# Kernel optimization log

Measured on AMD Instinct MI355X. Metric: run time of the kernel, lower is better.

## Reference

```python
import jax, jax.numpy as jnp
import numpy as np

B, S, D = 2, 2048, 1024
H = 2048          # expert hidden size; up-proj width is 2*H (GLU)
E = 8             # num_experts
K = 2             # top_k


def setup_inputs() -> dict:
    key = jax.random.key(0)
    k1, k2, k3, k4, k5 = jax.random.split(key, 5)
    x = jax.random.normal(k1, (B, S, D), dtype=jnp.float32)
    expert_p = jax.random.uniform(k2, (B, S, K), dtype=jnp.float32)
    expert_idxs = jax.random.randint(k3, (B, S, K), 0, E)
    W1 = jax.random.normal(k4, (E, D, 2 * H), dtype=jnp.float32) * 0.02
    W2 = jax.random.normal(k5, (E, H, D), dtype=jnp.float32) * 0.02
    return {"x": x, "expert_p": expert_p, "expert_idxs": expert_idxs, "W1": W1, "W2": W2}


def reference(x, expert_p, expert_idxs, W1, W2):
    # x: [B, S, D]; expert_p/expert_idxs: [B, S, K]; W1: [E, D, 2H]; W2: [E, H, D]
    x_shape = x.shape
    d = x_shape[-1]
    k = expert_idxs.shape[-1]
    n_experts = W1.shape[0]
    xf = x.reshape(-1, d)                      # [T, D]
    T = xf.shape[0]
    e_flat = expert_idxs.reshape(-1)           # [P] token-major pair order, P = T*k
    xp = jnp.repeat(xf, k, axis=0)             # [P, D] matches e_flat ordering

    # Grouped up-projection: each (token, expert) pair hits its expert's W1.
    up = jnp.zeros((T * k, W1.shape[-1]), dtype=x.dtype)
    for e in range(n_experts):                 # fixed small loop over experts
        up = up + jnp.where((e_flat == e)[:, None], xp @ W1[e], 0)

    # Fused GLU: chunk(2), exact GELU (torch nn.GELU default), gate (g + 1).
    h, g = jnp.split(up, 2, axis=-1)           # [P, H] each
    a = jax.nn.gelu(h, approximate=False) * (g + 1)

    # Grouped down-projection.
    down = jnp.zeros((T * k, d), dtype=x.dtype)
    for e in range(n_experts):
        down = down + jnp.where((e_flat == e)[:, None], a @ W2[e], 0)

    # Gated scatter-combine over the top_k pairs of each token.
    gates = expert_p.reshape(T, k)             # [T, K]
    y = jnp.sum(down.reshape(T, k, d) * gates[..., None], axis=1)
    return y.reshape(*x_shape[:-1], d)
```

## Files before the change

### kernel.cpp

```cpp
#include <hip/hip_runtime.h>
#include <hip/hip_bf16.h>
#include <math.h>

#define TT 4096
#define PP 8192
#define DD 1024
#define HH 2048
#define EE 8
#define CC1 4096

typedef __attribute__((ext_vector_type(8))) short s16x8;
typedef __attribute__((ext_vector_type(4))) float f32x4;

#define W1T_OFF   0ull
#define W2T_OFF   (W1T_OFF + (size_t)EE*DD*CC1*2)
#define XB_OFF    (W2T_OFF + (size_t)EE*HH*DD*2)
#define ABUF_OFF  (XB_OFF  + (size_t)TT*DD*2)
#define DOWN_OFF  (ABUF_OFF + (size_t)PP*HH*2)
#define META_OFF  (DOWN_OFF + (size_t)2*PP*DD*2)
#define PAIR_OFF  (META_OFF + 2048)
#define POS_OFF   (PAIR_OFF + (size_t)PP*4)

#define VMCNT(N) asm volatile("s_waitcnt vmcnt(" #N ")" ::: "memory")
#define CFENCE() asm volatile("" ::: "memory")

__device__ __forceinline__ unsigned short f2bf(float f) {
  union { float f; unsigned u; } a; a.f = f;
  unsigned u = a.u;
  unsigned r = u + 0x7FFFu + ((u >> 16) & 1u);
  return (unsigned short)(r >> 16);
}

__device__ __forceinline__ float bf2f(unsigned short s) {
  union { unsigned u; float f; } a; a.u = ((unsigned)s) << 16;
  return a.f;
}

__device__ __forceinline__ void gload16(const void* g, void* l) {
  __builtin_amdgcn_global_load_lds(
      (const __attribute__((address_space(1))) void*)(uintptr_t)g,
      (__attribute__((address_space(3))) void*)(unsigned)(uintptr_t)l,
      16, 0, 0);
}

__global__ void k_cvt_x(const float* __restrict__ in, unsigned short* __restrict__ out, int n4) {
  int i = blockIdx.x * blockDim.x + threadIdx.x;
  if (i >= n4) return;
  float4 v = reinterpret_cast<const float4*>(in)[i];
  ushort4 o;
  o.x = f2bf(v.x); o.y = f2bf(v.y); o.z = f2bf(v.z); o.w = f2bf(v.w);
  reinterpret_cast<ushort4*>(out)[i] = o;
}

__global__ __launch_bounds__(256) void k_transpose(const float* __restrict__ in,
                                                   unsigned short* __restrict__ out,
                                                   int R, int C) {
  __shared__ float t[64][65];
  const size_t mbase = (size_t)blockIdx.z * (size_t)R * (size_t)C;
  int c0 = blockIdx.x * 64, r0 = blockIdx.y * 64;
  int tid = threadIdx.x;
#pragma unroll
  for (int i = 0; i < 4; ++i) {
    int ch = tid + i * 256;
    int row = ch >> 4, c4 = (ch & 15) * 4;
    float4 v = *reinterpret_cast<const float4*>(&in[mbase + (size_t)(r0 + row) * C + c0 + c4]);
    t[row][c4] = v.x; t[row][c4 + 1] = v.y; t[row][c4 + 2] = v.z; t[row][c4 + 3] = v.w;
  }
  __syncthreads();
#pragma unroll
  for (int i = 0; i < 4; ++i) {
    int ch = tid + i * 256;
    int c = ch >> 4, rb = (ch & 15) * 4;
    ushort4 o;
    o.x = f2bf(t[rb][c]); o.y = f2bf(t[rb + 1][c]);
    o.z = f2bf(t[rb + 2][c]); o.w = f2bf(t[rb + 3][c]);
    *reinterpret_cast<ushort4*>(&out[mbase + (size_t)(c0 + c) * R + r0 + rb]) = o;
  }
}

__global__ void k_route(const int* __restrict__ eidx, int* __restrict__ meta,
                        int* __restrict__ plist, int* __restrict__ pos) {
  __shared__ int cnt[EE], off[EE + 1], cur[EE];
  int tid = threadIdx.x;
  if (tid < EE) { cnt[tid] = 0; cur[tid] = 0; }
  __syncthreads();
  for (int p = tid; p < PP; p += blockDim.x) atomicAdd(&cnt[eidx[p]], 1);
  __syncthreads();
  if (tid == 0) {
    int s = 0;
    for (int e = 0; e < EE; ++e) { off[e] = s; s += cnt[e]; }
    off[EE] = s;
    int n256 = 0;
    for (int e = 0; e < EE; ++e)
      for (int r = 0; r < cnt[e]; r += 256) {
        meta[16 + 2*n256] = e; meta[17 + 2*n256] = off[e] + r; ++n256;
      }
    meta[0] = n256;
    for (int e = 0; e <= EE; ++e) meta[1 + e] = off[e];
  }
  __syncthreads();
  for (int p = tid; p < PP; p += blockDim.x) {
    int e = eidx[p];
    int q = off[e] + atomicAdd(&cur[e], 1);
    plist[q] = p;
    pos[p] = q;
  }
}

__global__ __launch_bounds__(512) void k_gemm1(
    const unsigned short* __restrict__ xb,
    const unsigned short* __restrict__ w1t,
    const float* __restrict__ gates,
    const int* __restrict__ meta,
    const int* __restrict__ plist,
    unsigned short* __restrict__ abuf)
{
  const int nt = meta[0];
  const int tb = blockIdx.x;
  if (tb >= nt) return;
  const int e  = meta[16 + 2*tb];
  const int q0 = meta[17 + 2*tb];
  const int nrows = min(256, meta[2 + e] - q0);
  const int c0 = blockIdx.y * 64;

  __shared__ unsigned short As[3][256 * 64];
  __shared__ unsigned short Bs[3][128 * 64];

  const int tid = threadIdx.x;
  const int wave = tid >> 6, lane = tid & 63;
  const int l15 = lane & 15, l4 = lane >> 4;
  const int wr = wave >> 1, wc = wave & 1;

  const unsigned short* w1e = w1t + (size_t)e * CC1 * DD;

  const unsigned short* aga[4];
  const unsigned short* bga[2];
#pragma unroll
  for (int i = 0; i < 4; ++i) {
    int c = tid + i * 512;
    int row = c >> 3;
    int ko = ((c & 7) ^ (row & 7)) * 8;
    int r = row < nrows ? row : 0;
    int p = plist[q0 + r];
    aga[i] = xb + (size_t)(p >> 1) * DD + ko;
  }
#pragma unroll
  for (int i = 0; i < 2; ++i) {
    int c = tid + i * 512;
    int row = c >> 3;
    int ko = ((c & 7) ^ (row & 7)) * 8;
    int u = row & 63, wcq = row >> 6;
    int col = (u < 32) ? (c0 + wcq * 32 + u) : (HH + c0 + wcq * 32 + (u - 32));
    bga[i] = w1e + (size_t)col * DD + ko;
  }

  f32x4 acc[4][4];
#pragma unroll
  for (int a = 0; a < 4; ++a)
#pragma unroll
    for (int b = 0; b < 4; ++b) acc[a][b] = (f32x4)0.0f;

  auto stage = [&](int kk, unsigned short* pa, unsigned short* pb) {
#pragma unroll
    for (int i = 0; i < 4; ++i) gload16(aga[i] + kk, pa + (tid + i * 512) * 8);
#pragma unroll
    for (int i = 0; i < 2; ++i) gload16(bga[i] + kk, pb + (tid + i * 512) * 8);
  };

  auto compute_tile = [&](const unsigned short* sa, const unsigned short* sb) {
    const char* A8 = (const char*)sa;
    const char* B8 = (const char*)sb;
#pragma unroll
    for (int ks = 0; ks < 2; ++ks) {
      s16x8 af[4], bfr[4];
#pragma unroll
      for (int rf = 0; rf < 4; ++rf) {
        int row = wr * 64 + rf * 16 + l15;
        af[rf] = *(const s16x8*)(A8 + ((row * 128 + ks * 64 + l4 * 16) ^ ((row & 7) << 4)));
      }
#pragma unroll
      for (int cf = 0; cf < 4; ++cf) {
        int row = wc * 64 + cf * 16 + l15;
        bfr[cf] = *(const s16x8*)(B8 + ((row * 128 + ks * 64 + l4 * 16) ^ ((row & 7) << 4)));
      }
#pragma unroll
      for (int rf = 0; rf < 4; ++rf)
#pragma unroll
        for (int cf = 0; cf < 4; ++cf)
          acc[rf][cf] = __builtin_amdgcn_mfma_f32_16x16x32_bf16(af[rf], bfr[cf], acc[rf][cf], 0, 0, 0);
    }
  };

  unsigned short *a0 = As[0], *a1 = As[1], *a2 = As[2];
  unsigned short *b0 = Bs[0], *b1 = Bs[1], *b2 = Bs[2];

  stage(0, a0, b0);
  stage(64, a1, b1);
  VMCNT(6);
  __builtin_amdgcn_s_barrier();
  CFENCE();

  for (int kt = 0; kt < DD / 64 - 2; ++kt) {
    stage((kt + 2) * 64, a2, b2);
    compute_tile(a0, b0);
    VMCNT(6);
    __builtin_amdgcn_s_barrier();
    CFENCE();
    unsigned short* t;
    t = a0; a0 = a1; a1 = a2; a2 = t;
    t = b0; b0 = b1; b1 = b2; b2 = t;
  }
  compute_tile(a0, b0);
  VMCNT(0);
  __builtin_amdgcn_s_barrier();
  CFENCE();
  compute_tile(a1, b1);

#pragma unroll
  for (int rf = 0; rf < 4; ++rf) {
#pragma unroll
    for (int i = 0; i < 4; ++i) {
      int r = wr * 64 + rf * 16 + l4 * 4 + i;
      if (r < nrows) {
        int q = q0 + r;
        float gt = gates[plist[q]];
        unsigned short* orow = abuf + (size_t)q * HH + c0 + wc * 32 + l15;
#pragma unroll
        for (int cf = 0; cf < 2; ++cf) {
          float hv = acc[rf][cf][i];
          float gv = acc[rf][cf + 2][i];
          float av = 0.5f * hv * (1.0f + erff(hv * 0.70710678118654752f)) * (gv + 1.0f) * gt;
          orow[cf * 16] = f2bf(av);
        }
      }
    }
  }
}

__global__ __launch_bounds__(512) void k_gemm2(
    const unsigned short* __restrict__ abuf,
    const unsigned short* __restrict__ w2t,
    const int* __restrict__ meta,
    unsigned short* __restrict__ down)
{
  const int nt = meta[0];
  const int tb = blockIdx.x;
  if (tb >= nt) return;
  const int e  = meta[16 + 2*tb];
  const int q0 = meta[17 + 2*tb];
  const int nrows = min(256, meta[2 + e] - q0);
  const int c0 = blockIdx.y * 128;
  const int kz = blockIdx.z * (HH / 2);

  __shared__ unsigned short As[3][256 * 64];
  __shared__ unsigned short Bs[3][128 * 64];

  const int tid = threadIdx.x;
  const int wave = tid >> 6, lane = tid & 63;
  const int l15 = lane & 15, l4 = lane >> 4;
  const int wr = wave >> 1, wc = wave & 1;

  const unsigned short* w2e = w2t + (size_t)e * DD * HH;

  const unsigned short* aga[4];
  const unsigned short* bga[2];
#pragma unroll
  for (int i = 0; i < 4; ++i) {
    int c = tid + i * 512;
    int row = c >> 3;
    int ko = ((c & 7) ^ (row & 7)) * 8;
    int r = row < nrows ? row : 0;
    aga[i] = abuf + (size_t)(q0 + r) * HH + kz + ko;
  }
#pragma unroll
  for (int i = 0; i < 2; ++i) {
    int c = tid + i * 512;
    int row = c >> 3;
    int ko = ((c & 7) ^ (row & 7)) * 8;
    bga[i] = w2e + (size_t)(c0 + row) * HH + kz + ko;
  }

  f32x4 acc[4][4];
#pragma unroll
  for (int a = 0; a < 4; ++a)
#pragma unroll
    for (int b = 0; b < 4; ++b) acc[a][b] = (f32x4)0.0f;

  auto stage = [&](int kk, unsigned short* pa, unsigned short* pb) {
#pragma unroll
    for (int i = 0; i < 4; ++i) gload16(aga[i] + kk, pa + (tid + i * 512) * 8);
#pragma unroll
    for (int i = 0; i < 2; ++i) gload16(bga[i] + kk, pb + (tid + i * 512) * 8);
  };

  auto compute_tile = [&](const unsigned short* sa, const unsigned short* sb) {
    const char* A8 = (const char*)sa;
    const char* B8 = (const char*)sb;
#pragma unroll
    for (int ks = 0; ks < 2; ++ks) {
      s16x8 af[4], bfr[4];
#pragma unroll
      for (int rf = 0; rf < 4; ++rf) {
        int row = wr * 64 + rf * 16 + l15;
        af[rf] = *(const s16x8*)(A8 + ((row * 128 + ks * 64 + l4 * 16) ^ ((row & 7) << 4)));
      }
#pragma unroll
      for (int cf = 0; cf < 4; ++cf) {
        int row = wc * 64 + cf * 16 + l15;
        bfr[cf] = *(const s16x8*)(B8 + ((row * 128 + ks * 64 + l4 * 16) ^ ((row & 7) << 4)));
      }
#pragma unroll
      for (int rf = 0; rf < 4; ++rf)
#pragma unroll
        for (int cf = 0; cf < 4; ++cf)
          acc[rf][cf] = __builtin_amdgcn_mfma_f32_16x16x32_bf16(af[rf], bfr[cf], acc[rf][cf], 0, 0, 0);
    }
  };

  unsigned short *a0 = As[0], *a1 = As[1], *a2 = As[2];
  unsigned short *b0 = Bs[0], *b1 = Bs[1], *b2 = Bs[2];

  stage(0, a0, b0);
  stage(64, a1, b1);
  VMCNT(6);
  __builtin_amdgcn_s_barrier();
  CFENCE();

  const int NT = (HH / 2) / 64;
  for (int kt = 0; kt < NT - 2; ++kt) {
    stage((kt + 2) * 64, a2, b2);
    compute_tile(a0, b0);
    VMCNT(6);
    __builtin_amdgcn_s_barrier();
    CFENCE();
    unsigned short* t;
    t = a0; a0 = a1; a1 = a2; a2 = t;
    t = b0; b0 = b1; b1 = b2; b2 = t;
  }
  compute_tile(a0, b0);
  VMCNT(0);
  __builtin_amdgcn_s_barrier();
  CFENCE();
  compute_tile(a1, b1);

  unsigned short* dz = down + (size_t)blockIdx.z * PP * DD;
#pragma unroll
  for (int rf = 0; rf < 4; ++rf) {
#pragma unroll
    for (int i = 0; i < 4; ++i) {
      int r = wr * 64 + rf * 16 + l4 * 4 + i;
      if (r < nrows) {
        int q = q0 + r;
        unsigned short* orow = dz + (size_t)q * DD + c0 + wc * 64 + l15;
#pragma unroll
        for (int cf = 0; cf < 4; ++cf) orow[cf * 16] = f2bf(acc[rf][cf][i]);
      }
    }
  }
}

__global__ void k_combine(const unsigned short* __restrict__ down, const int* __restrict__ pos,
                          float* __restrict__ y) {
  int i = blockIdx.x * blockDim.x + threadIdx.x;
  if (i >= TT * DD / 8) return;
  int t = i >> 7;
  int c8 = (i & 127) * 8;
  int qa = pos[2 * t], qb = pos[2 * t + 1];
  const unsigned short* d0 = down;
  const unsigned short* d1 = down + (size_t)PP * DD;
  s16x8 va0 = *reinterpret_cast<const s16x8*>(d0 + (size_t)qa * DD + c8);
  s16x8 va1 = *reinterpret_cast<const s16x8*>(d1 + (size_t)qa * DD + c8);
  s16x8 vb0 = *reinterpret_cast<const s16x8*>(d0 + (size_t)qb * DD + c8);
  s16x8 vb1 = *reinterpret_cast<const s16x8*>(d1 + (size_t)qb * DD + c8);
  float o[8];
#pragma unroll
  for (int j = 0; j < 8; ++j)
    o[j] = bf2f((unsigned short)va0[j]) + bf2f((unsigned short)va1[j]) +
           bf2f((unsigned short)vb0[j]) + bf2f((unsigned short)vb1[j]);
  float4* yo = reinterpret_cast<float4*>(y + (size_t)t * DD + c8);
  yo[0] = (float4){o[0], o[1], o[2], o[3]};
  yo[1] = (float4){o[4], o[5], o[6], o[7]};
}

extern "C" void kernel_launch(void* const* d_in, const int* in_sizes, int n_in,
                              void* d_out, int out_size, void* d_ws, size_t ws_size,
                              hipStream_t stream) {
  const float* x  = (const float*)d_in[0];
  const float* ep = (const float*)d_in[1];
  const int*   ei = (const int*)d_in[2];
  const float* W1 = (const float*)d_in[3];
  const float* W2 = (const float*)d_in[4];
  float* y = (float*)d_out;
  char* ws = (char*)d_ws;

  unsigned short* w1t = (unsigned short*)(ws + W1T_OFF);
  unsigned short* w2t = (unsigned short*)(ws + W2T_OFF);
  unsigned short* xb  = (unsigned short*)(ws + XB_OFF);
  unsigned short* ab  = (unsigned short*)(ws + ABUF_OFF);
  unsigned short* down = (unsigned short*)(ws + DOWN_OFF);
  int* meta   = (int*)(ws + META_OFF);
  int* plist  = (int*)(ws + PAIR_OFF);
  int* pos    = (int*)(ws + POS_OFF);

  hipLaunchKernelGGL(k_cvt_x, dim3(TT * DD / 4 / 256), dim3(256), 0, stream,
                     x, xb, TT * DD / 4);
  hipLaunchKernelGGL(k_transpose, dim3(CC1 / 64, DD / 64, EE), dim3(256), 0, stream,
                     W1, w1t, DD, CC1);
  hipLaunchKernelGGL(k_transpose, dim3(DD / 64, HH / 64, EE), dim3(256), 0, stream,
                     W2, w2t, HH, DD);
  hipLaunchKernelGGL(k_route, dim3(1), dim3(256), 0, stream, ei, meta, plist, pos);
  hipLaunchKernelGGL(k_gemm1, dim3(40, 32), dim3(512), 0, stream,
                     xb, w1t, ep, meta, plist, ab);
  hipLaunchKernelGGL(k_gemm2, dim3(40, 8, 2), dim3(512), 0, stream,
                     ab, w2t, meta, down);
  hipLaunchKernelGGL(k_combine, dim3(TT * DD / 8 / 256), dim3(256), 0, stream,
                     down, pos, y);
}
```

Measured before the change: 270.1 us.

## Interleave LDS reads, global prefetch and MFMA in ping-pong phases with setprio

Both grouped GEMM kernels now split each K-tile into two half-phases. Each phase issues LDS fragment reads and half of the next tile's global-to-LDS loads, then waits at a barrier and on lgkmcnt before running 16 MFMAs under raised wave priority. The intent is a HipKittens-style ping-pong schedule in which some waves do memory work while others compute, keeping the matrix cores busier. It adds more barriers per tile, and the vmcnt(6) accounting must still line up with the split staging.

Result: no change. 275.0 us (+1.8%).

```diff
diff --git a/kernel.cpp b/kernel.cpp
--- a/kernel.cpp
+++ b/kernel.cpp
@@ -23,6 +23,8 @@
 
 #define VMCNT(N) asm volatile("s_waitcnt vmcnt(" #N ")" ::: "memory")
 #define CFENCE() asm volatile("" ::: "memory")
+#define LGKM0() do { asm volatile("s_waitcnt lgkmcnt(0)" ::: "memory"); \
+                     __builtin_amdgcn_sched_barrier(0); } while (0)
 
 __device__ __forceinline__ unsigned short f2bf(float f) {
   union { float f; unsigned u; } a; a.f = f;
@@ -160,61 +162,89 @@
 #pragma unroll
     for (int b = 0; b < 4; ++b) acc[a][b] = (f32x4)0.0f;
 
-  auto stage = [&](int kk, unsigned short* pa, unsigned short* pb) {
-#pragma unroll
-    for (int i = 0; i < 4; ++i) gload16(aga[i] + kk, pa + (tid + i * 512) * 8);
-#pragma unroll
-    for (int i = 0; i < 2; ++i) gload16(bga[i] + kk, pb + (tid + i * 512) * 8);
-  };
-
-  auto compute_tile = [&](const unsigned short* sa, const unsigned short* sb) {
+  auto stage_h0 = [&](int kk, unsigned short* pa, unsigned short* pb) {
+    gload16(aga[0] + kk, pa + (tid + 0 * 512) * 8);
+    gload16(aga[1] + kk, pa + (tid + 1 * 512) * 8);
+    gload16(bga[0] + kk, pb + (tid + 0 * 512) * 8);
+  };
+  auto stage_h1 = [&](int kk, unsigned short* pa, unsigned short* pb) {
+    gload16(aga[2] + kk, pa + (tid + 2 * 512) * 8);
+    gload16(aga[3] + kk, pa + (tid + 3 * 512) * 8);
+    gload16(bga[1] + kk, pb + (tid + 1 * 512) * 8);
+  };
+
+  auto dsread = [&](const unsigned short* sa, const unsigned short* sb, int ks,
+                    s16x8* af, s16x8* bfr) {
     const char* A8 = (const char*)sa;
     const char* B8 = (const char*)sb;
 #pragma unroll
-    for (int ks = 0; ks < 2; ++ks) {
-      s16x8 af[4], bfr[4];
-#pragma unroll
-      for (int rf = 0; rf < 4; ++rf) {
-        int row = wr * 64 + rf * 16 + l15;
-        af[rf] = *(const s16x8*)(A8 + ((row * 128 + ks * 64 + l4 * 16) ^ ((row & 7) << 4)));
-      }
-#pragma unroll
-      for (int cf = 0; cf < 4; ++cf) {
-        int row = wc * 64 + cf * 16 + l15;
-        bfr[cf] = *(const s16x8*)(B8 + ((row * 128 + ks * 64 + l4 * 16) ^ ((row & 7) << 4)));
-      }
-#pragma unroll
-      for (int rf = 0; rf < 4; ++rf)
-#pragma unroll
-        for (int cf = 0; cf < 4; ++cf)
-          acc[rf][cf] = __builtin_amdgcn_mfma_f32_16x16x32_bf16(af[rf], bfr[cf], acc[rf][cf], 0, 0, 0);
-    }
+    for (int rf = 0; rf < 4; ++rf) {
+      int row = wr * 64 + rf * 16 + l15;
+      af[rf] = *(const s16x8*)(A8 + ((row * 128 + ks * 64 + l4 * 16) ^ ((row & 7) << 4)));
+    }
+#pragma unroll
+    for (int cf = 0; cf < 4; ++cf) {
+      int row = wc * 64 + cf * 16 + l15;
+      bfr[cf] = *(const s16x8*)(B8 + ((row * 128 + ks * 64 + l4 * 16) ^ ((row & 7) << 4)));
+    }
+  };
+  auto mfma16 = [&](const s16x8* af, const s16x8* bfr) {
+    __builtin_amdgcn_s_setprio(1);
+#pragma unroll
+    for (int rf = 0; rf < 4; ++rf)
+#pragma unroll
+      for (int cf = 0; cf < 4; ++cf)
+        acc[rf][cf] = __builtin_amdgcn_mfma_f32_16x16x32_bf16(af[rf], bfr[cf], acc[rf][cf], 0, 0, 0);
+    __builtin_amdgcn_s_setprio(0);
   };
 
   unsigned short *a0 = As[0], *a1 = As[1], *a2 = As[2];
   unsigned short *b0 = Bs[0], *b1 = Bs[1], *b2 = Bs[2];
 
-  stage(0, a0, b0);
-  stage(64, a1, b1);
+  stage_h0(0, a0, b0);  stage_h1(0, a0, b0);
+  stage_h0(64, a1, b1); stage_h1(64, a1, b1);
   VMCNT(6);
   __builtin_amdgcn_s_barrier();
   CFENCE();
 
+  s16x8 af[4], bfr[4];
   for (int kt = 0; kt < DD / 64 - 2; ++kt) {
-    stage((kt + 2) * 64, a2, b2);
-    compute_tile(a0, b0);
+    const int kk = (kt + 2) * 64;
+    dsread(a0, b0, 0, af, bfr);
+    stage_h0(kk, a2, b2);
+    __builtin_amdgcn_s_barrier();
+    LGKM0();
+    mfma16(af, bfr);
+    __builtin_amdgcn_s_barrier();
+    dsread(a0, b0, 1, af, bfr);
+    stage_h1(kk, a2, b2);
     VMCNT(6);
+    __builtin_amdgcn_s_barrier();
+    LGKM0();
+    mfma16(af, bfr);
     __builtin_amdgcn_s_barrier();
     CFENCE();
     unsigned short* t;
     t = a0; a0 = a1; a1 = a2; a2 = t;
     t = b0; b0 = b1; b1 = b2; b2 = t;
   }
-  compute_tile(a0, b0);
+  dsread(a0, b0, 0, af, bfr);
+  __builtin_amdgcn_s_barrier();
+  LGKM0();
+  mfma16(af, bfr);
+  __builtin_amdgcn_s_barrier();
+  dsread(a0, b0, 1, af, bfr);
   VMCNT(0);
   __builtin_amdgcn_s_barrier();
-  CFENCE();
-  compute_tile(a1, b1);
+  LGKM0();
+  mfma16(af, bfr);
+  __builtin_amdgcn_s_barrier();
+  dsread(a1, b1, 0, af, bfr);
+  LGKM0();
+  mfma16(af, bfr);
+  dsread(a1, b1, 1, af, bfr);
+  LGKM0();
+  mfma16(af, bfr);
 
 #pragma unroll
   for (int rf = 0; rf < 4; ++rf) {
@@ -286,62 +316,89 @@
 #pragma unroll
     for (int b = 0; b < 4; ++b) acc[a][b] = (f32x4)0.0f;
 
-  auto stage = [&](int kk, unsigned short* pa, unsigned short* pb) {
-#pragma unroll
-    for (int i = 0; i < 4; ++i) gload16(aga[i] + kk, pa + (tid + i * 512) * 8);
-#pragma unroll
-    for (int i = 0; i < 2; ++i) gload16(bga[i] + kk, pb + (tid + i * 512) * 8);
-  };
-
-  auto compute_tile = [&](const unsigned short* sa, const unsigned short* sb) {
+  auto stage_h0 = [&](int kk, unsigned short* pa, unsigned short* pb) {
+    gload16(aga[0] + kk, pa + (tid + 0 * 512) * 8);
+    gload16(aga[1] + kk, pa + (tid + 1 * 512) * 8);
+    gload16(bga[0] + kk, pb + (tid + 0 * 512) * 8);
+  };
+  auto stage_h1 = [&](int kk, unsigned short* pa, unsigned short* pb) {
+    gload16(aga[2] + kk, pa + (tid + 2 * 512) * 8);
+    gload16(aga[3] + kk, pa + (tid + 3 * 512) * 8);
+    gload16(bga[1] + kk, pb + (tid + 1 * 512) * 8);
+  };
+  auto dsread = [&](const unsigned short* sa, const unsigned short* sb, int ks,
+                    s16x8* af, s16x8* bfr) {
     const char* A8 = (const char*)sa;
     const char* B8 = (const char*)sb;
 #pragma unroll
-    for (int ks = 0; ks < 2; ++ks) {
-      s16x8 af[4], bfr[4];
-#pragma unroll
-      for (int rf = 0; rf < 4; ++rf) {
-        int row = wr * 64 + rf * 16 + l15;
-        af[rf] = *(const s16x8*)(A8 + ((row * 128 + ks * 64 + l4 * 16) ^ ((row & 7) << 4)));
-      }
-#pragma unroll
-      for (int cf = 0; cf < 4; ++cf) {
-        int row = wc * 64 + cf * 16 + l15;
-        bfr[cf] = *(const s16x8*)(B8 + ((row * 128 + ks * 64 + l4 * 16) ^ ((row & 7) << 4)));
-      }
-#pragma unroll
-      for (int rf = 0; rf < 4; ++rf)
-#pragma unroll
-        for (int cf = 0; cf < 4; ++cf)
-          acc[rf][cf] = __builtin_amdgcn_mfma_f32_16x16x32_bf16(af[rf], bfr[cf], acc[rf][cf], 0, 0, 0);
-    }
+    for (int rf = 0; rf < 4; ++rf) {
+      int row = wr * 64 + rf * 16 + l15;
+      af[rf] = *(const s16x8*)(A8 + ((row * 128 + ks * 64 + l4 * 16) ^ ((row & 7) << 4)));
+    }
+#pragma unroll
+    for (int cf = 0; cf < 4; ++cf) {
+      int row = wc * 64 + cf * 16 + l15;
+      bfr[cf] = *(const s16x8*)(B8 + ((row * 128 + ks * 64 + l4 * 16) ^ ((row & 7) << 4)));
+    }
+  };
+  auto mfma16 = [&](const s16x8* af, const s16x8* bfr) {
+    __builtin_amdgcn_s_setprio(1);
+#pragma unroll
+    for (int rf = 0; rf < 4; ++rf)
+#pragma unroll
+      for (int cf = 0; cf < 4; ++cf)
+        acc[rf][cf] = __builtin_amdgcn_mfma_f32_16x16x32_bf16(af[rf], bfr[cf], acc[rf][cf], 0, 0, 0);
+    __builtin_amdgcn_s_setprio(0);
   };
 
   unsigned short *a0 = As[0], *a1 = As[1], *a2 = As[2];
   unsigned short *b0 = Bs[0], *b1 = Bs[1], *b2 = Bs[2];
 
-  stage(0, a0, b0);
-  stage(64, a1, b1);
+  stage_h0(0, a0, b0);  stage_h1(0, a0, b0);
+  stage_h0(64, a1, b1); stage_h1(64, a1, b1);
   VMCNT(6);
   __builtin_amdgcn_s_barrier();
   CFENCE();
 
+  s16x8 af[4], bfr[4];
   const int NT = (HH / 2) / 64;
   for (int kt = 0; kt < NT - 2; ++kt) {
-    stage((kt + 2) * 64, a2, b2);
-    compute_tile(a0, b0);
+    const int kk = (kt + 2) * 64;
+    dsread(a0, b0, 0, af, bfr);
+    stage_h0(kk, a2, b2);
+    __builtin_amdgcn_s_barrier();
+    LGKM0();
+    mfma16(af, bfr);
+    __builtin_amdgcn_s_barrier();
+    dsread(a0, b0, 1, af, bfr);
+    stage_h1(kk, a2, b2);
     VMCNT(6);
+    __builtin_amdgcn_s_barrier();
+    LGKM0();
+    mfma16(af, bfr);
     __builtin_amdgcn_s_barrier();
     CFENCE();
     unsigned short* t;
     t = a0; a0 = a1; a1 = a2; a2 = t;
     t = b0; b0 = b1; b1 = b2; b2 = t;
   }
-  compute_tile(a0, b0);
+  dsread(a0, b0, 0, af, bfr);
+  __builtin_amdgcn_s_barrier();
+  LGKM0();
+  mfma16(af, bfr);
+  __builtin_amdgcn_s_barrier();
+  dsread(a0, b0, 1, af, bfr);
   VMCNT(0);
   __builtin_amdgcn_s_barrier();
-  CFENCE();
-  compute_tile(a1, b1);
+  LGKM0();
+  mfma16(af, bfr);
+  __builtin_amdgcn_s_barrier();
+  dsread(a1, b1, 0, af, bfr);
+  LGKM0();
+  mfma16(af, bfr);
+  dsread(a1, b1, 1, af, bfr);
+  LGKM0();
+  mfma16(af, bfr);
 
   unsigned short* dz = down + (size_t)blockIdx.z * PP * DD;
 #pragma unroll
```

## Enlarge grouped-GEMM tiles to 256x256, double-buffer, and split down-proj K four ways

Applied to the files above, without the earlier changes.

Both expert GEMMs move from 256x128 to 256x256 output tiles, with each wave owning a 128x64 sub-tile. The goal is to raise arithmetic intensity and cut redundant global loads of the activation rows. The triple-buffered vmcnt-pipelined loop becomes a simpler double-buffered loop that uses __syncthreads, which can expose more load latency. The down-projection split-K goes from 2 to 4 so the grid size stays the same, and the combine kernel now sums four partials. To fit the larger partial buffer, it reuses the W1 transpose workspace after gemm1 has finished. The 128KB LDS per block and 128 accumulator floats per thread, together with launch_bounds(512,2), risk register spills and low occupancy.

New measurement: 282.9 us. 4.7% more time.

```diff
diff --git a/kernel.cpp b/kernel.cpp
--- a/kernel.cpp
+++ b/kernel.cpp
@@ -13,16 +13,13 @@
 typedef __attribute__((ext_vector_type(4))) float f32x4;
 
 #define W1T_OFF   0ull
+#define DOWN_OFF  W1T_OFF
 #define W2T_OFF   (W1T_OFF + (size_t)EE*DD*CC1*2)
 #define XB_OFF    (W2T_OFF + (size_t)EE*HH*DD*2)
 #define ABUF_OFF  (XB_OFF  + (size_t)TT*DD*2)
-#define DOWN_OFF  (ABUF_OFF + (size_t)PP*HH*2)
-#define META_OFF  (DOWN_OFF + (size_t)2*PP*DD*2)
+#define META_OFF  (ABUF_OFF + (size_t)PP*HH*2)
 #define PAIR_OFF  (META_OFF + 2048)
 #define POS_OFF   (PAIR_OFF + (size_t)PP*4)
-
-#define VMCNT(N) asm volatile("s_waitcnt vmcnt(" #N ")" ::: "memory")
-#define CFENCE() asm volatile("" ::: "memory")
 
 __device__ __forceinline__ unsigned short f2bf(float f) {
   union { float f; unsigned u; } a; a.f = f;
@@ -107,7 +104,7 @@
   }
 }
 
-__global__ __launch_bounds__(512) void k_gemm1(
+__global__ __launch_bounds__(512, 2) void k_gemm1(
     const unsigned short* __restrict__ xb,
     const unsigned short* __restrict__ w1t,
     const float* __restrict__ gates,
@@ -121,20 +118,20 @@
   const int e  = meta[16 + 2*tb];
   const int q0 = meta[17 + 2*tb];
   const int nrows = min(256, meta[2 + e] - q0);
-  const int c0 = blockIdx.y * 64;
-
-  __shared__ unsigned short As[3][256 * 64];
-  __shared__ unsigned short Bs[3][128 * 64];
+  const int c0 = blockIdx.y * 128;
+
+  __shared__ unsigned short As[2][256 * 64];
+  __shared__ unsigned short Bs[2][256 * 64];
 
   const int tid = threadIdx.x;
   const int wave = tid >> 6, lane = tid & 63;
   const int l15 = lane & 15, l4 = lane >> 4;
-  const int wr = wave >> 1, wc = wave & 1;
+  const int wm = wave >> 2, wn = wave & 3;
 
   const unsigned short* w1e = w1t + (size_t)e * CC1 * DD;
 
   const unsigned short* aga[4];
-  const unsigned short* bga[2];
+  const unsigned short* bga[4];
 #pragma unroll
   for (int i = 0; i < 4; ++i) {
     int c = tid + i * 512;
@@ -143,20 +140,14 @@
     int r = row < nrows ? row : 0;
     int p = plist[q0 + r];
     aga[i] = xb + (size_t)(p >> 1) * DD + ko;
-  }
-#pragma unroll
-  for (int i = 0; i < 2; ++i) {
-    int c = tid + i * 512;
-    int row = c >> 3;
-    int ko = ((c & 7) ^ (row & 7)) * 8;
-    int u = row & 63, wcq = row >> 6;
-    int col = (u < 32) ? (c0 + wcq * 32 + u) : (HH + c0 + wcq * 32 + (u - 32));
+    int b = row >> 4, u = row & 15;
+    int col = ((b & 1) ? HH : 0) + c0 + (b >> 1) * 16 + u;
     bga[i] = w1e + (size_t)col * DD + ko;
   }
 
-  f32x4 acc[4][4];
-#pragma unroll
-  for (int a = 0; a < 4; ++a)
+  f32x4 acc[8][4];
+#pragma unroll
+  for (int a = 0; a < 8; ++a)
 #pragma unroll
     for (int b = 0; b < 4; ++b) acc[a][b] = (f32x4)0.0f;
 
@@ -164,7 +155,7 @@
 #pragma unroll
     for (int i = 0; i < 4; ++i) gload16(aga[i] + kk, pa + (tid + i * 512) * 8);
 #pragma unroll
-    for (int i = 0; i < 2; ++i) gload16(bga[i] + kk, pb + (tid + i * 512) * 8);
+    for (int i = 0; i < 4; ++i) gload16(bga[i] + kk, pb + (tid + i * 512) * 8);
   };
 
   auto compute_tile = [&](const unsigned short* sa, const unsigned short* sb) {
@@ -172,72 +163,56 @@
     const char* B8 = (const char*)sb;
 #pragma unroll
     for (int ks = 0; ks < 2; ++ks) {
-      s16x8 af[4], bfr[4];
-#pragma unroll
-      for (int rf = 0; rf < 4; ++rf) {
-        int row = wr * 64 + rf * 16 + l15;
+      s16x8 af[8], bfr[4];
+#pragma unroll
+      for (int rf = 0; rf < 8; ++rf) {
+        int row = wm * 128 + rf * 16 + l15;
         af[rf] = *(const s16x8*)(A8 + ((row * 128 + ks * 64 + l4 * 16) ^ ((row & 7) << 4)));
       }
 #pragma unroll
       for (int cf = 0; cf < 4; ++cf) {
-        int row = wc * 64 + cf * 16 + l15;
+        int row = wn * 64 + cf * 16 + l15;
         bfr[cf] = *(const s16x8*)(B8 + ((row * 128 + ks * 64 + l4 * 16) ^ ((row & 7) << 4)));
       }
 #pragma unroll
-      for (int rf = 0; rf < 4; ++rf)
+      for (int rf = 0; rf < 8; ++rf)
 #pragma unroll
         for (int cf = 0; cf < 4; ++cf)
           acc[rf][cf] = __builtin_amdgcn_mfma_f32_16x16x32_bf16(af[rf], bfr[cf], acc[rf][cf], 0, 0, 0);
     }
   };
 
-  unsigned short *a0 = As[0], *a1 = As[1], *a2 = As[2];
-  unsigned short *b0 = Bs[0], *b1 = Bs[1], *b2 = Bs[2];
-
-  stage(0, a0, b0);
-  stage(64, a1, b1);
-  VMCNT(6);
-  __builtin_amdgcn_s_barrier();
-  CFENCE();
-
-  for (int kt = 0; kt < DD / 64 - 2; ++kt) {
-    stage((kt + 2) * 64, a2, b2);
-    compute_tile(a0, b0);
-    VMCNT(6);
-    __builtin_amdgcn_s_barrier();
-    CFENCE();
-    unsigned short* t;
-    t = a0; a0 = a1; a1 = a2; a2 = t;
-    t = b0; b0 = b1; b1 = b2; b2 = t;
-  }
-  compute_tile(a0, b0);
-  VMCNT(0);
-  __builtin_amdgcn_s_barrier();
-  CFENCE();
-  compute_tile(a1, b1);
-
-#pragma unroll
-  for (int rf = 0; rf < 4; ++rf) {
+  stage(0, As[0], Bs[0]);
+  __syncthreads();
+  const int NT = DD / 64;
+  for (int kt = 0; kt < NT; ++kt) {
+    if (kt + 1 < NT) stage((kt + 1) * 64, As[(kt + 1) & 1], Bs[(kt + 1) & 1]);
+    compute_tile(As[kt & 1], Bs[kt & 1]);
+    if (kt + 1 < NT) __syncthreads();
+  }
+
+#pragma unroll
+  for (int rf = 0; rf < 8; ++rf) {
 #pragma unroll
     for (int i = 0; i < 4; ++i) {
-      int r = wr * 64 + rf * 16 + l4 * 4 + i;
+      int r = wm * 128 + rf * 16 + l4 * 4 + i;
       if (r < nrows) {
         int q = q0 + r;
         float gt = gates[plist[q]];
-        unsigned short* orow = abuf + (size_t)q * HH + c0 + wc * 32 + l15;
-#pragma unroll
-        for (int cf = 0; cf < 2; ++cf) {
-          float hv = acc[rf][cf][i];
-          float gv = acc[rf][cf + 2][i];
+        unsigned short* orow = abuf + (size_t)q * HH + c0 + 2 * wn * 16 + l15;
+#pragma unroll
+        for (int j = 0; j < 2; ++j) {
+          float hv = acc[rf][2 * j][i];
+          float gv = acc[rf][2 * j + 1][i];
           float av = 0.5f * hv * (1.0f + erff(hv * 0.70710678118654752f)) * (gv + 1.0f) * gt;
-          orow[cf * 16] = f2bf(av);
+          orow[j * 16] = f2bf(av);
         }
       }
     }
   }
 }
 
-__global__ __launch_bounds__(512) void k_gemm2(
+__global__ __launch_bounds__(512, 2) void k_gemm2(
     const unsigned short* __restrict__ abuf,
     const unsigned short* __restrict__ w2t,
     const int* __restrict__ meta,
@@ -249,21 +224,21 @@
   const int e  = meta[16 + 2*tb];
   const int q0 = meta[17 + 2*tb];
   const int nrows = min(256, meta[2 + e] - q0);
-  const int c0 = blockIdx.y * 128;
-  const int kz = blockIdx.z * (HH / 2);
-
-  __shared__ unsigned short As[3][256 * 64];
-  __shared__ unsigned short Bs[3][128 * 64];
+  const int c0 = blockIdx.y * 256;
+  const int kz = blockIdx.z * (HH / 4);
+
+  __shared__ unsigned short As[2][256 * 64];
+  __shared__ unsigned short Bs[2][256 * 64];
 
   const int tid = threadIdx.x;
   const int wave = tid >> 6, lane = tid & 63;
   const int l15 = lane & 15, l4 = lane >> 4;
-  const int wr = wave >> 1, wc = wave & 1;
+  const int wm = wave >> 2, wn = wave & 3;
 
   const unsigned short* w2e = w2t + (size_t)e * DD * HH;
 
   const unsigned short* aga[4];
-  const unsigned short* bga[2];
+  const unsigned short* bga[4];
 #pragma unroll
   for (int i = 0; i < 4; ++i) {
     int c = tid + i * 512;
@@ -271,18 +246,12 @@
     int ko = ((c & 7) ^ (row & 7)) * 8;
     int r = row < nrows ? row : 0;
     aga[i] = abuf + (size_t)(q0 + r) * HH + kz + ko;
-  }
-#pragma unroll
-  for (int i = 0; i < 2; ++i) {
-    int c = tid + i * 512;
-    int row = c >> 3;
-    int ko = ((c & 7) ^ (row & 7)) * 8;
     bga[i] = w2e + (size_t)(c0 + row) * HH + kz + ko;
   }
 
-  f32x4 acc[4][4];
-#pragma unroll
-  for (int a = 0; a < 4; ++a)
+  f32x4 acc[8][4];
+#pragma unroll
+  for (int a = 0; a < 8; ++a)
 #pragma unroll
     for (int b = 0; b < 4; ++b) acc[a][b] = (f32x4)0.0f;
 
@@ -290,7 +259,7 @@
 #pragma unroll
     for (int i = 0; i < 4; ++i) gload16(aga[i] + kk, pa + (tid + i * 512) * 8);
 #pragma unroll
-    for (int i = 0; i < 2; ++i) gload16(bga[i] + kk, pb + (tid + i * 512) * 8);
+    for (int i = 0; i < 4; ++i) gload16(bga[i] + kk, pb + (tid + i * 512) * 8);
   };
 
   auto compute_tile = [&](const unsigned short* sa, const unsigned short* sb) {
@@ -298,60 +267,43 @@
     const char* B8 = (const char*)sb;
 #pragma unroll
     for (int ks = 0; ks < 2; ++ks) {
-      s16x8 af[4], bfr[4];
-#pragma unroll
-      for (int rf = 0; rf < 4; ++rf) {
-        int row = wr * 64 + rf * 16 + l15;
+      s16x8 af[8], bfr[4];
+#pragma unroll
+      for (int rf = 0; rf < 8; ++rf) {
+        int row = wm * 128 + rf * 16 + l15;
         af[rf] = *(const s16x8*)(A8 + ((row * 128 + ks * 64 + l4 * 16) ^ ((row & 7) << 4)));
       }
 #pragma unroll
       for (int cf = 0; cf < 4; ++cf) {
-        int row = wc * 64 + cf * 16 + l15;
+        int row = wn * 64 + cf * 16 + l15;
         bfr[cf] = *(const s16x8*)(B8 + ((row * 128 + ks * 64 + l4 * 16) ^ ((row & 7) << 4)));
       }
 #pragma unroll
-      for (int rf = 0; rf < 4; ++rf)
+      for (int rf = 0; rf < 8; ++rf)
 #pragma unroll
         for (int cf = 0; cf < 4; ++cf)
           acc[rf][cf] = __builtin_amdgcn_mfma_f32_16x16x32_bf16(af[rf], bfr[cf], acc[rf][cf], 0, 0, 0);
     }
   };
 
-  unsigned short *a0 = As[0], *a1 = As[1], *a2 = As[2];
-  unsigned short *b0 = Bs[0], *b1 = Bs[1], *b2 = Bs[2];
-
-  stage(0, a0, b0);
-  stage(64, a1, b1);
-  VMCNT(6);
-  __builtin_amdgcn_s_barrier();
-  CFENCE();
-
-  const int NT = (HH / 2) / 64;
-  for (int kt = 0; kt < NT - 2; ++kt) {
-    stage((kt + 2) * 64, a2, b2);
-    compute_tile(a0, b0);
-    VMCNT(6);
-    __builtin_amdgcn_s_barrier();
-    CFENCE();
-    unsigned short* t;
-    t = a0; a0 = a1; a1 = a2; a2 = t;
-    t = b0; b0 = b1; b1 = b2; b2 = t;
-  }
-  compute_tile(a0, b0);
-  VMCNT(0);
-  __builtin_amdgcn_s_barrier();
-  CFENCE();
-  compute_tile(a1, b1);
+  stage(0, As[0], Bs[0]);
+  __syncthreads();
+  const int NT = (HH / 4) / 64;
+  for (int kt = 0; kt < NT; ++kt) {
+    if (kt + 1 < NT) stage((kt + 1) * 64, As[(kt + 1) & 1], Bs[(kt + 1) & 1]);
+    compute_tile(As[kt & 1], Bs[kt & 1]);
+    if (kt + 1 < NT) __syncthreads();
+  }
 
   unsigned short* dz = down + (size_t)blockIdx.z * PP * DD;
 #pragma unroll
-  for (int rf = 0; rf < 4; ++rf) {
+  for (int rf = 0; rf < 8; ++rf) {
 #pragma unroll
     for (int i = 0; i < 4; ++i) {
-      int r = wr * 64 + rf * 16 + l4 * 4 + i;
+      int r = wm * 128 + rf * 16 + l4 * 4 + i;
       if (r < nrows) {
         int q = q0 + r;
-        unsigned short* orow = dz + (size_t)q * DD + c0 + wc * 64 + l15;
+        unsigned short* orow = dz + (size_t)q * DD + c0 + wn * 64 + l15;
 #pragma unroll
         for (int cf = 0; cf < 4; ++cf) orow[cf * 16] = f2bf(acc[rf][cf][i]);
       }
@@ -366,17 +318,18 @@
   int t = i >> 7;
   int c8 = (i & 127) * 8;
   int qa = pos[2 * t], qb = pos[2 * t + 1];
-  const unsigned short* d0 = down;
-  const unsigned short* d1 = down + (size_t)PP * DD;
-  s16x8 va0 = *reinterpret_cast<const s16x8*>(d0 + (size_t)qa * DD + c8);
-  s16x8 va1 = *reinterpret_cast<const s16x8*>(d1 + (size_t)qa * DD + c8);
-  s16x8 vb0 = *reinterpret_cast<const s16x8*>(d0 + (size_t)qb * DD + c8);
-  s16x8 vb1 = *reinterpret_cast<const s16x8*>(d1 + (size_t)qb * DD + c8);
   float o[8];
 #pragma unroll
-  for (int j = 0; j < 8; ++j)
-    o[j] = bf2f((unsigned short)va0[j]) + bf2f((unsigned short)va1[j]) +
-           bf2f((unsigned short)vb0[j]) + bf2f((unsigned short)vb1[j]);
+  for (int j = 0; j < 8; ++j) o[j] = 0.0f;
+#pragma unroll
+  for (int z = 0; z < 4; ++z) {
+    const unsigned short* dz = down + (size_t)z * PP * DD;
+    s16x8 va = *reinterpret_cast<const s16x8*>(dz + (size_t)qa * DD + c8);
+    s16x8 vb = *reinterpret_cast<const s16x8*>(dz + (size_t)qb * DD + c8);
+#pragma unroll
+    for (int j = 0; j < 8; ++j)
+      o[j] += bf2f((unsigned short)va[j]) + bf2f((unsigned short)vb[j]);
+  }
   float4* yo = reinterpret_cast<float4*>(y + (size_t)t * DD + c8);
   yo[0] = (float4){o[0], o[1], o[2], o[3]};
   yo[1] = (float4){o[4], o[5], o[6], o[7]};
@@ -409,9 +362,9 @@
   hipLaunchKernelGGL(k_transpose, dim3(DD / 64, HH / 64, EE), dim3(256), 0, stream,
                      W2, w2t, HH, DD);
   hipLaunchKernelGGL(k_route, dim3(1), dim3(256), 0, stream, ei, meta, plist, pos);
-  hipLaunchKernelGGL(k_gemm1, dim3(40, 32), dim3(512), 0, stream,
+  hipLaunchKernelGGL(k_gemm1, dim3(40, 16), dim3(512), 0, stream,
                      xb, w1t, ep, meta, plist, ab);
-  hipLaunchKernelGGL(k_gemm2, dim3(40, 8, 2), dim3(512), 0, stream,
+  hipLaunchKernelGGL(k_gemm2, dim3(40, 4, 4), dim3(512), 0, stream,
                      ab, w2t, meta, down);
   hipLaunchKernelGGL(k_combine, dim3(TT * DD / 8 / 256), dim3(256), 0, stream,
                      down, pos, y);
```
